# Kernel tuning notes

Hardware: AMD Instinct MI355X
Metric: run time of the kernel (lower is better)

The kernel has to match this reference:

```python
import jax, jax.numpy as jnp
import numpy as np

NUM_HEADS = 16
D_MODEL = 1024
HEAD_DIM = D_MODEL // NUM_HEADS
SOFTCAP = 50.0
MAX_WAVELENGTH = 10000.0
B, S = 2, 2048


def apply_rope(x, positions, head_dim):
    # x: [B, S, H, head_dim], positions: [B, S]
    fraction = 2.0 * jnp.arange(head_dim // 2, dtype=jnp.float32) / head_dim
    timescale = MAX_WAVELENGTH ** fraction                      # [hd/2]
    sinusoid = positions[..., None].astype(jnp.float32) / timescale  # [B,S,hd/2]
    sinusoid = sinusoid[..., None, :]                           # [B,S,1,hd/2]
    sin, cos = jnp.sin(sinusoid), jnp.cos(sinusoid)
    first, second = jnp.split(x, 2, axis=-1)
    return jnp.concatenate([first * cos - second * sin,
                            second * cos + first * sin], axis=-1).astype(x.dtype)


def setup_inputs() -> dict:
    key = jax.random.key(0)
    k1, k2, k3 = jax.random.split(key, 3)
    inputs = jax.random.normal(k1, (B, S, D_MODEL), dtype=jnp.float32)
    segment_positions = jnp.tile(jnp.arange(S, dtype=jnp.int32)[None, :], (B, 1))
    # causal mask, broadcast over heads: [B, 1, S, S]
    mask = jnp.tril(jnp.ones((S, S), dtype=bool))[None, None, :, :]
    mask = jnp.broadcast_to(mask, (B, 1, S, S))
    w_in = jax.random.normal(k2, (D_MODEL, NUM_HEADS, 3 * HEAD_DIM), dtype=jnp.float32) * 0.02
    w_out = jax.random.normal(k3, (NUM_HEADS, HEAD_DIM, D_MODEL), dtype=jnp.float32) * 0.02
    return {"inputs": inputs, "segment_positions": segment_positions,
            "mask": mask, "w_in": w_in, "w_out": w_out}


def reference(inputs, segment_positions, mask, w_in, w_out):
    # fused QKV projection: [B,S,H,3*hd]
    in_proj = jnp.einsum('bsd,dhf->bshf', inputs, w_in)
    query, key, value = jnp.split(in_proj, 3, axis=-1)       # each [B,S,H,hd]
    query = apply_rope(query, segment_positions, HEAD_DIM)
    key = apply_rope(key, segment_positions, HEAD_DIM)
    query = query / jnp.sqrt(jnp.float32(HEAD_DIM))
    attn = jnp.einsum('bqhd,bkhd->bhqk', query, key)          # [B,H,S,S]
    big_neg = jnp.finfo(jnp.float32).min
    attn = jnp.where(mask, attn, big_neg)
    attn = jnp.tanh(attn / SOFTCAP) * SOFTCAP                 # logit softcap
    attn = jax.nn.softmax(attn, axis=-1)
    x = jnp.einsum('bhqk,bkhd->bqhd', attn, value)            # [B,S,H,hd]
    out = jnp.einsum('bqhd,hdm->bqm', x, w_out)               # [B,S,D]
    return out
```

## Files before the change

kernel.cpp:

```cpp
#include <hip/hip_runtime.h>
#include <hip/hip_bf16.h>

typedef unsigned short u16;
typedef __attribute__((ext_vector_type(8))) short short8;
typedef __attribute__((ext_vector_type(2))) float f32x2;
typedef __attribute__((ext_vector_type(4))) float f32x4;
typedef __attribute__((ext_vector_type(16))) float f32x16;

#define NH 16
#define HD 64
#define SEQ 2048
#define NBATCH 2
#define DM 1024

#define GLOAD_LDS(g, l)                                                              \
  __builtin_amdgcn_global_load_lds((__attribute__((address_space(1))) const void*)(g), \
                                   (__attribute__((address_space(3))) void*)(l), 16, 0, 0)

__device__ __forceinline__ u16 f2bf(float f) {
  __hip_bfloat16 h = __float2bfloat16(f);
  return *reinterpret_cast<u16*>(&h);
}
__device__ __forceinline__ float bf2f(u16 u) {
  union { unsigned int i; float f; } v; v.i = ((unsigned int)u) << 16; return v.f;
}
__device__ __forceinline__ f32x4 mfma16(short8 a, short8 b, f32x4 c) {
  return __builtin_amdgcn_mfma_f32_16x16x32_bf16(a, b, c, 0, 0, 0);
}
__device__ __forceinline__ f32x16 mfma32(short8 a, short8 b, f32x16 c) {
  return __builtin_amdgcn_mfma_f32_32x32x16_bf16(a, b, c, 0, 0, 0);
}

__global__ __launch_bounds__(256) void k_prep(const float* __restrict__ inputs,
                                              u16* __restrict__ Xbf,
                                              const float* __restrict__ w_in,
                                              u16* __restrict__ WinT,
                                              const float* __restrict__ w_out,
                                              u16* __restrict__ WoutT,
                                              float2* __restrict__ SC) {
  __shared__ float t[32][33];
  int blk = blockIdx.x, tid = threadIdx.x;
  if (blk < 4096) {
    int i = blk * 256 + tid;
    float4 v = reinterpret_cast<const float4*>(inputs)[i];
    union { u16 h[4]; unsigned long long u; } o;
    o.h[0] = f2bf(v.x); o.h[1] = f2bf(v.y); o.h[2] = f2bf(v.z); o.h[3] = f2bf(v.w);
    reinterpret_cast<unsigned long long*>(Xbf)[i] = o.u;
  } else if (blk < 4096 + 3072 + 1024) {
    const float* src; u16* dst; int C, bx, by;
    if (blk < 4096 + 3072) {
      int b2 = blk - 4096; src = w_in; dst = WinT; C = 3072; bx = b2 % 96; by = b2 / 96;
    } else {
      int b2 = blk - (4096 + 3072); src = w_out; dst = WoutT; C = 1024; bx = b2 & 31; by = b2 >> 5;
    }
    const int R = 1024;
    int c0 = bx * 32, r0 = by * 32;
    int tx = tid & 31, ty = tid >> 5;
#pragma unroll
    for (int i = 0; i < 4; ++i)
      t[ty + 8 * i][tx] = src[(size_t)(r0 + ty + 8 * i) * C + c0 + tx];
    __syncthreads();
#pragma unroll
    for (int i = 0; i < 4; ++i)
      dst[(size_t)(c0 + ty + 8 * i) * R + r0 + tx] = f2bf(t[tx][ty + 8 * i]);
  } else {
    int idx = (blk - 8192) * 256 + tid;
    int p = idx >> 5, i = idx & 31;
    const float l2ts = 0.41524101186092029f;
    float inv = exp2f(-(float)i * l2ts);
    float arg = (float)p * inv;
    float s, c;
    sincosf(arg, &s, &c);
    SC[idx] = make_float2(s, c);
  }
}

__global__ __launch_bounds__(256) void k_rope(u16* __restrict__ Q, const u16* __restrict__ Kraw,
                                              u16* __restrict__ Kf,
                                              const int* __restrict__ segpos,
                                              const float2* __restrict__ sc) {
  int blk = blockIdx.x, tid = threadIdx.x;
  if (blk < 256) {
    int r = blk * 256 + tid;
    int b = r >> 15;
    int s = r & (SEQ - 1);
    int pos = segpos[b * SEQ + s];
    const float2* scp = sc + (size_t)pos * 32;
    u16* row = Q + (size_t)r * HD;
    uint4 v[8];
#pragma unroll
    for (int i = 0; i < 8; ++i) v[i] = reinterpret_cast<uint4*>(row)[i];
    u16* e = reinterpret_cast<u16*>(v);
#pragma unroll
    for (int i = 0; i < 32; ++i) {
      float a = bf2f(e[i]), bq = bf2f(e[i + 32]);
      float2 t = scp[i];
      e[i] = f2bf((a * t.y - bq * t.x) * 0.125f);
      e[i + 32] = f2bf((bq * t.y + a * t.x) * 0.125f);
    }
#pragma unroll
    for (int i = 0; i < 8; ++i) reinterpret_cast<uint4*>(row)[i] = v[i];
  } else {
    int wid = (blk - 256) * 4 + (tid >> 6);
    int lane = tid & 63, ql = lane & 31, hi = lane >> 5;
#pragma unroll
    for (int t2 = 0; t2 < 2; ++t2) {
      int t = wid * 2 + t2;
      int bh = t >> 6, kt = t & 63;
      int b = bh >> 4;
      int r = kt * 32 + ql;
      int pos = segpos[b * SEQ + r];
      const u16* src = Kraw + ((size_t)bh * SEQ + r) * HD + hi * 8;
      short8 ch[4];
#pragma unroll
      for (int d0 = 0; d0 < 4; ++d0)
        ch[d0] = *reinterpret_cast<const short8*>(src + d0 * 16);
      const float2* scp = sc + (size_t)pos * 32 + hi * 8;
#pragma unroll
      for (int d0 = 0; d0 < 2; ++d0)
#pragma unroll
        for (int e = 0; e < 8; ++e) {
          float2 tt = scp[d0 * 16 + e];
          float a = bf2f(((u16*)&ch[d0])[e]);
          float bb = bf2f(((u16*)&ch[d0 + 2])[e]);
          ((u16*)&ch[d0])[e] = f2bf(a * tt.y - bb * tt.x);
          ((u16*)&ch[d0 + 2])[e] = f2bf(bb * tt.y + a * tt.x);
        }
      u16* dst = Kf + (size_t)bh * SEQ * HD + (size_t)kt * 2048 + lane * 8;
#pragma unroll
      for (int d0 = 0; d0 < 4; ++d0)
        *reinterpret_cast<short8*>(dst + d0 * 512) = ch[d0];
    }
  }
}

template <int MODE>
__global__ __launch_bounds__(256, 6) void k_gemm(const u16* __restrict__ A,
                                                 const u16* __restrict__ Bt,
                                                 int N, u16* __restrict__ q, u16* __restrict__ kk,
                                                 u16* __restrict__ vt, float* __restrict__ out) {
  __shared__ alignas(16) u16 As[64][64];
  __shared__ alignas(16) u16 Bs[64][64];
  const int K = 1024;
  int tid = threadIdx.x;
  int lane = tid & 63, w = tid >> 6;
  int wr = w >> 1, wc = w & 1;
  int col = lane & 15, grp = lane >> 4;
  int cx = col & 7;
  int bid = blockIdx.y * gridDim.x + blockIdx.x;
  int qq = (gridDim.x * gridDim.y) >> 3;
  int swz = (bid & 7) * qq + (bid >> 3);
  int m0 = (swz / gridDim.x) * 64;
  int n0 = (swz % gridDim.x) * 64;
  int crow = lane >> 3;
  int ccol = ((lane & 7) ^ (lane >> 3)) * 8;
  f32x4 zero4 = {0.f, 0.f, 0.f, 0.f};
  f32x4 acc[2][2];
#pragma unroll
  for (int i = 0; i < 2; ++i)
#pragma unroll
    for (int j = 0; j < 2; ++j) acc[i][j] = zero4;

  for (int k0 = 0; k0 < K; k0 += 64) {
    __syncthreads();
#pragma unroll
    for (int c = 0; c < 4; ++c) {
      int chunk = w * 4 + c;
      if (chunk < 8) {
        int r = chunk * 8 + crow;
        GLOAD_LDS(&A[(size_t)(m0 + r) * K + k0 + ccol], &As[0][0] + chunk * 512);
      } else {
        int r = (chunk - 8) * 8 + crow;
        GLOAD_LDS(&Bt[(size_t)(n0 + r) * K + k0 + ccol], &Bs[0][0] + (chunk - 8) * 512);
      }
    }
    __syncthreads();
#pragma unroll
    for (int kf = 0; kf < 2; ++kf) {
      short8 af[2], bfr[2];
      int sw = ((kf * 4 + grp) ^ cx) * 8;
#pragma unroll
      for (int i = 0; i < 2; ++i)
        af[i] = *reinterpret_cast<const short8*>(&As[wr * 32 + i * 16 + col][sw]);
#pragma unroll
      for (int i = 0; i < 2; ++i)
        bfr[i] = *reinterpret_cast<const short8*>(&Bs[wc * 32 + i * 16 + col][sw]);
#pragma unroll
      for (int mi = 0; mi < 2; ++mi)
#pragma unroll
        for (int ni = 0; ni < 2; ++ni) acc[mi][ni] = mfma16(af[mi], bfr[ni], acc[mi][ni]);
    }
  }
#pragma unroll
  for (int mi = 0; mi < 2; ++mi)
#pragma unroll
    for (int ni = 0; ni < 2; ++ni)
#pragma unroll
      for (int j = 0; j < 4; ++j) {
        int m = m0 + wr * 32 + mi * 16 + grp * 4 + j;
        int n = n0 + wc * 32 + ni * 16 + col;
        float v = acc[mi][ni][j];
        if (MODE == 0) {
          int b = m >> 11, s = m & 2047;
          int h = n / 192, f = n - h * 192;
          u16 bv = f2bf(v);
          if (f < 64)
            q[(((size_t)(b * NH + h) * SEQ + s) << 6) + f] = bv;
          else if (f < 128)
            kk[(((size_t)(b * NH + h) * SEQ + s) << 6) + (f - 64)] = bv;
          else {
            int d = f - 128, kv = s & 31;
            vt[(size_t)(b * NH + h) * (HD * SEQ) + (size_t)(s >> 5) * 2048 +
               ((kv >> 4) << 10) + ((d >> 5) << 9) + (((kv >> 3) & 1) << 8) +
               ((d & 31) << 3) + (kv & 7)] = bv;
          }
        } else {
          out[(size_t)m * N + n] = v;
        }
      }
}

#define TILE_BODY(KBASE, DIAG)                                                          \
  {                                                                                     \
    int kbase = (KBASE);                                                                \
    const u16* Ktile = Kb + (size_t)(kbase >> 5) * 2048;                                \
    short8 kf[4];                                                                       \
    _Pragma("unroll") for (int d0 = 0; d0 < 4; ++d0)                                    \
      kf[d0] = *reinterpret_cast<const short8*>(&Ktile[d0 * 512 + lane * 8]);           \
    f32x16 sacc;                                                                        \
    _Pragma("unroll") for (int r = 0; r < 16; ++r) sacc[r] = 0.f;                       \
    __builtin_amdgcn_s_setprio(1);                                                      \
    _Pragma("unroll") for (int d0 = 0; d0 < 4; ++d0) sacc = mfma32(kf[d0], qf[d0], sacc); \
    __builtin_amdgcn_s_setprio(0);                                                      \
    const u16* Vtile = Vb + (size_t)(kbase >> 5) * 2048;                                \
    short8 vf[2][2];                                                                    \
    _Pragma("unroll") for (int c = 0; c < 2; ++c)                                       \
      _Pragma("unroll") for (int dh = 0; dh < 2; ++dh)                                  \
        vf[c][dh] = *reinterpret_cast<const short8*>(                                   \
            &Vtile[(c * 2 + dh) * 512 + lane * 8]);                                     \
    float p[16];                                                                        \
    _Pragma("unroll") for (int r2 = 0; r2 < 8; ++r2) {                                  \
      f32x2 s2 = {sacc[2 * r2], sacc[2 * r2 + 1]};                                      \
      f32x2 t2 = s2 * s2;                                                               \
      f32x2 u2 = __builtin_elementwise_fma(t2, C52, C32);                               \
      u2 = __builtin_elementwise_fma(t2, u2, L2E2);                                     \
      f32x2 v2 = s2 * u2;                                                               \
      float p0 = __builtin_amdgcn_exp2f(v2.x);                                          \
      float p1 = __builtin_amdgcn_exp2f(v2.y);                                          \
      if (DIAG) {                                                                       \
        int r = 2 * r2;                                                                 \
        int kpos0 = kbase + (r & 3) + 8 * (r >> 2) + 4 * hi;                            \
        int kpos1 = kbase + ((r + 1) & 3) + 8 * ((r + 1) >> 2) + 4 * hi;                \
        if (kpos0 > qbase + ql) p0 = 0.f;                                               \
        if (kpos1 > qbase + ql) p1 = 0.f;                                               \
      }                                                                                 \
      p[2 * r2] = p0;                                                                   \
      p[2 * r2 + 1] = p1;                                                               \
      lsum2 += (f32x2){p0, p1};                                                         \
    }                                                                                   \
    short8 pfrag[2];                                                                    \
    _Pragma("unroll") for (int c = 0; c < 2; ++c) {                                     \
      unsigned int a0, a1, b0, b1;                                                      \
      asm("v_cvt_pk_bf16_f32 %0, %1, %2" : "=v"(a0) : "v"(p[8 * c + 0]), "v"(p[8 * c + 1])); \
      asm("v_cvt_pk_bf16_f32 %0, %1, %2" : "=v"(a1) : "v"(p[8 * c + 2]), "v"(p[8 * c + 3])); \
      asm("v_cvt_pk_bf16_f32 %0, %1, %2" : "=v"(b0) : "v"(p[8 * c + 4]), "v"(p[8 * c + 5])); \
      asm("v_cvt_pk_bf16_f32 %0, %1, %2" : "=v"(b1) : "v"(p[8 * c + 6]), "v"(p[8 * c + 7])); \
      asm("v_permlane32_swap_b32 %0, %1" : "+v"(a0), "+v"(b0));                         \
      asm("v_permlane32_swap_b32 %0, %1" : "+v"(a1), "+v"(b1));                         \
      union { unsigned int u[4]; short8 s8; } pk;                                       \
      pk.u[0] = a0; pk.u[1] = a1; pk.u[2] = b0; pk.u[3] = b1;                           \
      pfrag[c] = pk.s8;                                                                 \
    }                                                                                   \
    __builtin_amdgcn_s_setprio(1);                                                      \
    _Pragma("unroll") for (int c = 0; c < 2; ++c) {                                     \
      xacc0 = mfma32(pfrag[c], vf[c][0], xacc0);                                        \
      xacc1 = mfma32(pfrag[c], vf[c][1], xacc1);                                        \
    }                                                                                   \
    __builtin_amdgcn_s_setprio(0);                                                      \
  }

__global__ __launch_bounds__(256, 4) void k_attn(const u16* __restrict__ Q,
                                                 const u16* __restrict__ Kf,
                                                 const u16* __restrict__ Vt,
                                                 u16* __restrict__ X) {
  int lin = blockIdx.x;
  int xcd = lin & 7;
  int jj = lin >> 3;
  int bh = xcd * 4 + (jj & 3);
  int iq = jj >> 2;
  int tid = threadIdx.x, lane = tid & 63, w = tid >> 6;
  int ql = lane & 31, hi = lane >> 5;
  const u16* Qb = Q + (size_t)bh * SEQ * HD;
  const u16* Kb = Kf + (size_t)bh * SEQ * HD;
  const u16* Vb = Vt + (size_t)bh * HD * SEQ;
  int b = bh >> 4, h = bh & 15;
  size_t ob = (size_t)b * SEQ * DM + (size_t)h * HD;

  __shared__ float cbuf[3][64][34];

  const float L2E = 1.4426950408889634f;
  const f32x2 C32 = {-1.9235933878519513e-4f, -1.9235933878519513e-4f};
  const f32x2 C52 = {3.0777494205630686e-8f, 3.0777494205630686e-8f};
  const f32x2 L2E2 = {L2E, L2E};

  for (int half = 0; half < 2; ++half) {
    int qc = half ? iq : 63 - iq;
    int qbase = qc * 32;

    short8 qf[4];
#pragma unroll
    for (int d0 = 0; d0 < 4; ++d0)
      qf[d0] = *reinterpret_cast<const short8*>(&Qb[(size_t)(qbase + ql) * HD + d0 * 16 + hi * 8]);

    f32x16 xacc0, xacc1;
#pragma unroll
    for (int r = 0; r < 16; ++r) { xacc0[r] = 0.f; xacc1[r] = 0.f; }
    f32x2 lsum2 = {0.f, 0.f};

    for (int kt = w; kt < qc; kt += 4) TILE_BODY(kt * 32, false)
    if ((qc & 3) == w) TILE_BODY(qc * 32, true)

    float lsum = lsum2.x + lsum2.y;

    if (w > 0) {
#pragma unroll
      for (int r = 0; r < 16; ++r) {
        cbuf[w - 1][lane][r] = xacc0[r];
        cbuf[w - 1][lane][16 + r] = xacc1[r];
      }
      cbuf[w - 1][lane][32] = lsum;
    }
    __syncthreads();

    if (w == 0) {
#pragma unroll
      for (int s = 0; s < 3; ++s) {
#pragma unroll
        for (int r = 0; r < 16; ++r) {
          xacc0[r] += cbuf[s][lane][r];
          xacc1[r] += cbuf[s][lane][16 + r];
        }
        lsum += cbuf[s][lane][32];
      }
      lsum += __shfl_xor(lsum, 32, 64);
      float rinv = __builtin_amdgcn_rcpf(lsum);

#pragma unroll
      for (int r = 0; r < 16; ++r) {
        int qrel = (r & 3) + 8 * (r >> 2) + 4 * hi;
        float rv = __shfl(rinv, qrel, 64);
        size_t row = ob + (size_t)(qbase + qrel) * DM;
        X[row + ql] = f2bf(xacc0[r] * rv);
        X[row + 32 + ql] = f2bf(xacc1[r] * rv);
      }
    }
    __syncthreads();
  }
}

extern "C" void kernel_launch(void* const* d_in, const int* in_sizes, int n_in,
                              void* d_out, int out_size, void* d_ws, size_t ws_size,
                              hipStream_t stream) {
  const float* inputs = (const float*)d_in[0];
  const int* segpos = (const int*)d_in[1];
  const float* w_in = (const float*)d_in[3];
  const float* w_out = (const float*)d_in[4];
  float* out = (float*)d_out;
  char* ws = (char*)d_ws;

  size_t o = 0;
  u16* Xbf = (u16*)(ws + o); o += (size_t)4096 * 1024 * 2;
  u16* WinT = (u16*)(ws + o); o += (size_t)3072 * 1024 * 2;
  u16* WoutT = (u16*)(ws + o); o += (size_t)1024 * 1024 * 2;
  u16* Qb = (u16*)(ws + o); o += (size_t)NBATCH * NH * SEQ * HD * 2;
  u16* Kb = (u16*)(ws + o); o += (size_t)NBATCH * NH * SEQ * HD * 2;
  u16* Kf = (u16*)(ws + o); o += (size_t)NBATCH * NH * SEQ * HD * 2;
  u16* Vt = (u16*)(ws + o); o += (size_t)NBATCH * NH * HD * SEQ * 2;
  float2* SC = (float2*)(ws + o); o += (size_t)SEQ * 32 * sizeof(float2);

  k_prep<<<8448, 256, 0, stream>>>(inputs, Xbf, w_in, WinT, w_out, WoutT, SC);
  k_gemm<0><<<dim3(48, 64), 256, 0, stream>>>(Xbf, WinT, 3072, Qb, Kb, Vt, nullptr);
  k_rope<<<512, 256, 0, stream>>>(Qb, Kb, Kf, segpos, SC);
  k_attn<<<1024, 256, 0, stream>>>(Qb, Kf, Vt, Xbf);
  k_gemm<1><<<dim3(16, 64), 256, 0, stream>>>(Xbf, WoutT, 1024, nullptr, nullptr, nullptr, out);
}
```

Measured before the change: 115.6 us.

## Double-buffer LDS tiles in projection GEMM to overlap loads with MFMA

The QKV and output projection GEMM now allocates two LDS buffers for the A and B tiles. It issues the global-to-LDS loads for the next K-step before computing on the current one, so there is one barrier per step instead of two. The goal is to hide global load latency behind MFMA work. In exchange, LDS use per block doubles and the occupancy hint of 6 blocks per CU is dropped, which may reduce the number of resident blocks.

```diff
diff --git a/kernel.cpp b/kernel.cpp
--- a/kernel.cpp
+++ b/kernel.cpp
@@ -135,12 +135,12 @@
 }
 
 template <int MODE>
-__global__ __launch_bounds__(256, 6) void k_gemm(const u16* __restrict__ A,
-                                                 const u16* __restrict__ Bt,
-                                                 int N, u16* __restrict__ q, u16* __restrict__ kk,
-                                                 u16* __restrict__ vt, float* __restrict__ out) {
-  __shared__ alignas(16) u16 As[64][64];
-  __shared__ alignas(16) u16 Bs[64][64];
+__global__ __launch_bounds__(256) void k_gemm(const u16* __restrict__ A,
+                                              const u16* __restrict__ Bt,
+                                              int N, u16* __restrict__ q, u16* __restrict__ kk,
+                                              u16* __restrict__ vt, float* __restrict__ out) {
+  __shared__ alignas(16) u16 As[2][64][64];
+  __shared__ alignas(16) u16 Bs[2][64][64];
   const int K = 1024;
   int tid = threadIdx.x;
   int lane = tid & 63, w = tid >> 6;
@@ -154,6 +154,22 @@
   int n0 = (swz % gridDim.x) * 64;
   int crow = lane >> 3;
   int ccol = ((lane & 7) ^ (lane >> 3)) * 8;
+
+#define STAGE(BUF, K0)                                                                  \
+  {                                                                                     \
+    _Pragma("unroll") for (int c = 0; c < 4; ++c) {                                     \
+      int chunk = w * 4 + c;                  \
+      if (chunk < 8) {                                                                  \
+        int r = chunk * 8 + crow;                                                       \
+        GLOAD_LDS(&A[(size_t)(m0 + r) * K + (K0) + ccol], &As[BUF][0][0] + chunk * 512);\
+      } else {                                                                          \
+        int r = (chunk - 8) * 8 + crow;                                                 \
+        GLOAD_LDS(&Bt[(size_t)(n0 + r) * K + (K0) + ccol],                              \
+                  &Bs[BUF][0][0] + (chunk - 8) * 512);                                  \
+      }                                                                                 \
+    }                                                                                   \
+  }
+
   f32x4 zero4 = {0.f, 0.f, 0.f, 0.f};
   f32x4 acc[2][2];
 #pragma unroll
@@ -161,36 +177,34 @@
 #pragma unroll
     for (int j = 0; j < 2; ++j) acc[i][j] = zero4;
 
-  for (int k0 = 0; k0 < K; k0 += 64) {
-    __syncthreads();
-#pragma unroll
-    for (int c = 0; c < 4; ++c) {
-      int chunk = w * 4 + c;
-      if (chunk < 8) {
-        int r = chunk * 8 + crow;
-        GLOAD_LDS(&A[(size_t)(m0 + r) * K + k0 + ccol], &As[0][0] + chunk * 512);
-      } else {
-        int r = (chunk - 8) * 8 + crow;
-        GLOAD_LDS(&Bt[(size_t)(n0 + r) * K + k0 + ccol], &Bs[0][0] + (chunk - 8) * 512);
-      }
-    }
-    __syncthreads();
+  STAGE(0, 0)
+  __syncthreads();
+
+  int cur = 0;
+  for (int step = 0; step < 16; ++step) {
+    if (step < 15) STAGE(cur ^ 1, (step + 1) * 64)
 #pragma unroll
     for (int kf = 0; kf < 2; ++kf) {
       short8 af[2], bfr[2];
       int sw = ((kf * 4 + grp) ^ cx) * 8;
 #pragma unroll
       for (int i = 0; i < 2; ++i)
-        af[i] = *reinterpret_cast<const short8*>(&As[wr * 32 + i * 16 + col][sw]);
+        af[i] = *reinterpret_cast<const short8*>(&As[cur][wr * 32 + i * 16 + col][sw]);
 #pragma unroll
       for (int i = 0; i < 2; ++i)
-        bfr[i] = *reinterpret_cast<const short8*>(&Bs[wc * 32 + i * 16 + col][sw]);
+        bfr[i] = *reinterpret_cast<const short8*>(&Bs[cur][wc * 32 + i * 16 + col][sw]);
 #pragma unroll
       for (int mi = 0; mi < 2; ++mi)
 #pragma unroll
         for (int ni = 0; ni < 2; ++ni) acc[mi][ni] = mfma16(af[mi], bfr[ni], acc[mi][ni]);
     }
-  }
+    if (step < 15) {
+      __syncthreads();
+      cur ^= 1;
+    }
+  }
+#undef STAGE
+
 #pragma unroll
   for (int mi = 0; mi < 2; ++mi)
 #pragma unroll
```

Measured after the change: 118.8 us. +2.8%, slower.
